# Kernel optimization log

Measured on AMD Instinct MI355X. Metric: run time of the kernel, lower is better.

Reference implementation:

```python
import jax, jax.numpy as jnp
import numpy as np

N = 128   # image_size == proj_size
C = 16    # channels
B = 1
NUM_AP = 1
AP_ANGLES = np.linspace(0.0, 0.0, NUM_AP).tolist()
APLT_ANGLES = np.linspace(0.0, np.pi / 2, 2).tolist()
EPS = 1e-5


def _conv3d(x, w, b):
    # x: [B,C,D,H,W], w: [O,I,3,3,3]
    y = jax.lax.conv_general_dilated(
        x, w, window_strides=(1, 1, 1), padding='SAME',
        dimension_numbers=('NCDHW', 'OIDHW', 'NCDHW'))
    return y + b[None, :, None, None, None]


def _instance_norm(x):
    # InstanceNorm3d, affine=False: normalize per (batch, channel) over D,H,W
    m = x.mean(axis=(2, 3, 4), keepdims=True)
    v = x.var(axis=(2, 3, 4), keepdims=True)
    return (x - m) * jax.lax.rsqrt(v + EPS)


def _resblock(x, w1, b1, w2, b2):
    out = jax.nn.relu(_instance_norm(_conv3d(x, w1, b1)))
    out = _instance_norm(_conv3d(out, w2, b2)) + x
    return jax.nn.relu(out)


def _backproject(proj):
    # proj: [B,C,A,Z,U] -> volume [B,C,Z,N,N] (parallel-beam smear-back)
    c = (N - 1) / 2.0
    ys, xs = jnp.meshgrid(jnp.arange(N, dtype=jnp.float32),
                          jnp.arange(N, dtype=jnp.float32), indexing='ij')
    vol = jnp.zeros((proj.shape[0], proj.shape[1], proj.shape[3], N, N), proj.dtype)
    for a, th in enumerate(AP_ANGLES):
        u = np.cos(th) * (ys - c) + np.sin(th) * (xs - c) + c  # [N,N] detector coord
        u0 = jnp.clip(jnp.floor(u).astype(jnp.int32), 0, N - 2)
        w = u - u0.astype(u.dtype)
        p = proj[:, :, a]                     # [B,C,Z,U]
        g = p[..., u0] * (1.0 - w) + p[..., u0 + 1] * w   # [B,C,Z,N,N]
        valid = (u >= 0.0) & (u <= N - 1.0)
        vol = vol + jnp.where(valid, g, 0.0)
    return vol / float(len(AP_ANGLES))


def _forward_project(vol):
    # vol: [B,C,Z,H,W] -> proj [B,C,A,Z,U] (line integrals per z-slice)
    c = (N - 1) / 2.0
    uu, tt = jnp.meshgrid(jnp.arange(N, dtype=jnp.float32),
                          jnp.arange(N, dtype=jnp.float32), indexing='ij')
    projs = []
    for th in APLT_ANGLES:
        y = c + (uu - c) * np.cos(th) - (tt - c) * np.sin(th)
        x = c + (uu - c) * np.sin(th) + (tt - c) * np.cos(th)
        y0 = jnp.clip(jnp.floor(y).astype(jnp.int32), 0, N - 2)
        x0 = jnp.clip(jnp.floor(x).astype(jnp.int32), 0, N - 2)
        wy = y - y0.astype(y.dtype)
        wx = x - x0.astype(x.dtype)
        g = (vol[:, :, :, y0, x0] * (1 - wy) * (1 - wx)
             + vol[:, :, :, y0 + 1, x0] * wy * (1 - wx)
             + vol[:, :, :, y0, x0 + 1] * (1 - wy) * wx
             + vol[:, :, :, y0 + 1, x0 + 1] * wy * wx)   # [B,C,Z,U,T]
        valid = (y >= 0.0) & (y <= N - 1.0) & (x >= 0.0) & (x <= N - 1.0)
        projs.append(jnp.where(valid, g, 0.0).sum(axis=-1))  # sum over ray param t
    return jnp.stack(projs, axis=2)  # [B,C,A,Z,U]


def setup_inputs() -> dict:
    key = jax.random.key(0)
    ks = jax.random.split(key, 9)
    scale = 1.0 / np.sqrt(C * 27)
    inp = {'projection_data': jax.random.normal(ks[0], (B, C, NUM_AP, N, N), jnp.float32)}
    for i, name in enumerate(['a1', 'a2', 'b1', 'b2']):
        inp['w_' + name] = jax.random.normal(ks[1 + 2 * i], (C, C, 3, 3, 3), jnp.float32) * scale
        inp['b_' + name] = jax.random.normal(ks[2 + 2 * i], (C,), jnp.float32) * 0.01
    return inp


def reference(projection_data, w_a1, b_a1, w_a2, b_a2, w_b1, b_b1, w_b2, b_b2):
    vol = _backproject(projection_data)
    vol = _resblock(vol, w_a1, b_a1, w_a2, b_a2)
    vol = _resblock(vol, w_b1, b_b1, w_b2, b_b2)
    return _forward_project(vol)
```

## Files before the change

### kernel.cpp

```cpp
#include <hip/hip_runtime.h>


typedef unsigned short u16;
typedef unsigned int   u32;
using s16x8 = __attribute__((ext_vector_type(8))) short;
using f32x4 = __attribute__((ext_vector_type(4))) float;

#define IN_ELEMS 262144
#define MN_ELEMS 4194304
#define WS_NEED  28505408ull

__device__ __forceinline__ float bf2f(u16 h) {
    union { u32 u; float f; } v; v.u = ((u32)h) << 16; return v.f;
}
__device__ __forceinline__ u16 f2bf(float f) {
    union { float f; u32 u; } v; v.f = f;
    u32 u = v.u;
    return (u16)((u + 0x7fffu + ((u >> 16) & 1u)) >> 16);
}
__device__ __forceinline__ float ldin(const void* p, int i, int bf) {
    return bf ? bf2f(((const u16*)p)[i]) : ((const float*)p)[i];
}
__device__ __forceinline__ u16 ldbf(const void* p, int i, int bf) {
    return bf ? ((const u16*)p)[i] : f2bf(((const float*)p)[i]);
}
__device__ __forceinline__ void unpack8(uint4 a, float* f) {
    u32 w[4] = {a.x, a.y, a.z, a.w};
#pragma unroll
    for (int i = 0; i < 4; i++) {
        f[2*i]   = bf2f((u16)(w[i] & 0xffff));
        f[2*i+1] = bf2f((u16)(w[i] >> 16));
    }
}
__device__ __forceinline__ void unpack4(uint2 a, float* f) {
    f[0] = bf2f((u16)(a.x & 0xffff)); f[1] = bf2f((u16)(a.x >> 16));
    f[2] = bf2f((u16)(a.y & 0xffff)); f[3] = bf2f((u16)(a.y >> 16));
}

__global__ void sentinel_k(u16* __restrict__ out, int n)
{
    int i = blockIdx.x * 256 + threadIdx.x;
    if (i < n) out[i] = 0x4640;
}

__global__ __launch_bounds__(256) void wprep_prep_k(
    const void* __restrict__ w0, const void* __restrict__ w1,
    const void* __restrict__ w2, const void* __restrict__ w3,
    const void* __restrict__ b0, const void* __restrict__ b1,
    const void* __restrict__ b2, const void* __restrict__ b3,
    const void* __restrict__ proj,
    float* __restrict__ st, int* __restrict__ flag,
    float* __restrict__ biasf, float* __restrict__ w2d,
    float* __restrict__ pz, u16* __restrict__ afrag,
    float* __restrict__ I0, u16* __restrict__ M0)
{
    const int tid = threadIdx.x;
    const u16* pp = (const u16*)w0;
    int cnt = 0;
    for (int i = 0; i < 32; i++) {
        int e = (pp[2 * i] >> 7) & 0xFF;
        if (e >= 64 && e <= 130) cnt++;
    }
    const int bf = (cnt >= 24) ? 1 : 0;
    const void* WS[4] = {w0, w1, w2, w3};
    const void* BS[4] = {b0, b1, b2, b3};
    const int b = blockIdx.x;

    if (b >= 135) {
        const int bb = b - 135;
        const int d = bb >> 2;
        const int ys = (bb & 3) * 32;
        for (int i = tid; i < 512; i += 256) {
            int y = ys + (i >> 4), c = i & 15;
            I0[(d * 128 + y) * 16 + c] = ldin(proj, c * 16384 + d * 128 + y, bf);
        }
        for (int i = tid; i < 1024; i += 256) {
            int y = ys + (i >> 5), x = (i >> 1) & 15, hh = i & 1;
            bool on = (x <= 4) | (x == 7) | (x >= 8 && x < 12);
            u32 pw[4] = {0u, 0u, 0u, 0u};
            if (on) {
#pragma unroll
                for (int j = 0; j < 4; j++) {
                    int c0 = hh * 8 + 2 * j;
                    u16 a = f2bf(ldin(proj, c0 * 16384 + d * 128 + y, bf));
                    u16 bb2 = f2bf(ldin(proj, (c0 + 1) * 16384 + d * 128 + y, bf));
                    pw[j] = (u32)a | ((u32)bb2 << 16);
                }
            }
            *(uint4*)(M0 + ((d * 128 + y) << 8) + (x << 4) + hh * 8) =
                make_uint4(pw[0], pw[1], pw[2], pw[3]);
        }
        return;
    }

    if (b < 18) {
        int gi = b * 256 + tid;
        int L = gi / 1152, r = gi - L * 1152;
        int fi = r >> 6, l = r & 63;
        int kzky = fi >> 1, grp = fi & 1;
        int kz = kzky / 3, ky = kzky % 3;
        int n = l & 15, g = l >> 4, h = g & 1, kxs = g >> 1;
        int kx = grp * 2 + kxs;
        u16 v[8];
#pragma unroll
        for (int e = 0; e < 8; e++) {
            int ci = h * 8 + e;
            v[e] = (kx <= 2) ? ldbf(WS[L], n * 432 + ci * 27 + kz * 9 + ky * 3 + kx, bf)
                             : (u16)0;
        }
#pragma unroll
        for (int e = 0; e < 8; e++) afrag[gi * 8 + e] = v[e];
    } else if (b == 18) {
        st[tid] = 0.f;
        if (tid == 0) *flag = bf;
        if (tid < 64) biasf[tid] = ldin(BS[tid >> 4], tid & 15, bf);
    } else if (b < 99) {
        int i = (b - 19) * 256 + tid;
        pz[i] = 0.f;
    } else {
        int gi = (b - 99) * 256 + tid;
        int L = gi / 2304, r = gi - L * 2304;
        int tap = r >> 8, ci = (r >> 4) & 15, co = r & 15;
        int kz = tap / 3, ky = tap % 3;
        float s = 0.f;
#pragma unroll
        for (int kx = 0; kx < 3; kx++)
            s += ldin(WS[L], (co * 16 + ci) * 27 + kz * 9 + ky * 3 + kx, bf);
        w2d[gi] = s;
    }
}

__global__ __launch_bounds__(256) void layer_k(
    const float* __restrict__ Iin, const u16* __restrict__ Min,
    const float* __restrict__ w2dL, const u16* __restrict__ afragL,
    const float* __restrict__ biasL,
    float* __restrict__ Iout, u16* __restrict__ Mout,
    float* __restrict__ st_out)
{
    __shared__ __align__(16) char smem_raw[27776];
    const int tid = threadIdx.x;

    if (blockIdx.x < 256) {
        float* smem = (float*)smem_raw;
        float* wsl  = smem;
        float* pin  = smem + 2304;
        float* sred = smem + 5670;
        const int d  = blockIdx.x >> 1;
        const int y0 = (blockIdx.x & 1) * 64;
        if (tid < 32) sred[tid] = 0.f;
        for (int i = tid; i < 2304; i += 256) wsl[i] = w2dL[i];
        for (int i = tid; i < 3168; i += 256) {
            int p = i / 1056, r = i - p * 1056;
            int row = r >> 4, c = r & 15;
            int zz = d + p - 1, gy = y0 + row - 1;
            float v = 0.f;
            if ((unsigned)zz < 128u && (unsigned)gy < 128u)
                v = Iin[(zz * 128 + gy) * 16 + c];
            pin[p * 1122 + row * 17 + c] = v;
        }
        __syncthreads();

        const int yl = tid & 63, h = tid >> 6;
        float acc[4];
#pragma unroll
        for (int cc = 0; cc < 4; cc++) acc[cc] = biasL[h * 4 + cc];
#pragma unroll
        for (int kz = 0; kz < 3; kz++) {
#pragma unroll
            for (int ky = 0; ky < 3; ky++) {
                const float* rowb = &pin[kz * 1122 + (yl + ky) * 17];
                const float* wrow = &wsl[(kz * 3 + ky) * 256 + h * 4];
#pragma unroll
                for (int ci = 0; ci < 16; ci++) {
                    float v = rowb[ci];
#pragma unroll
                    for (int cc = 0; cc < 4; cc++)
                        acc[cc] = fmaf(v, wrow[ci * 16 + cc], acc[cc]);
                }
            }
        }
        const int e = (d * 128 + y0 + yl) * 16 + h * 4;
        *(float4*)(Iout + e) = make_float4(acc[0], acc[1], acc[2], acc[3]);
        float s[4], q[4];
#pragma unroll
        for (int cc = 0; cc < 4; cc++) { s[cc] = acc[cc]; q[cc] = acc[cc] * acc[cc]; }
#pragma unroll
        for (int off = 1; off < 64; off <<= 1) {
#pragma unroll
            for (int cc = 0; cc < 4; cc++) {
                s[cc] += __shfl_down(s[cc], off, 64);
                q[cc] += __shfl_down(q[cc], off, 64);
            }
        }
        if ((tid & 63) == 0) {
#pragma unroll
            for (int cc = 0; cc < 4; cc++) {
                atomicAdd(&sred[h * 4 + cc], s[cc]);
                atomicAdd(&sred[16 + h * 4 + cc], q[cc]);
            }
        }
        __syncthreads();
        if (tid < 32) atomicAdd(&st_out[tid], 120.f * sred[tid]);
        return;
    }

    u16*   stage = (u16*)smem_raw;
    float* sred  = (float*)(smem_raw + 27648);
    const int mb = blockIdx.x - 256;
    const int z  = mb & 127;
    const int yt = mb >> 7;
    const int l = tid & 63, w = tid >> 6;
    const int n = l & 15, g = l >> 4, h = g & 1, kxs = g >> 1;
    const int y0 = yt * 16 + w * 4;
    const int y0b = yt * 16;

    if (tid < 32) sred[tid] = 0.f;

    s16x8 af[18];
#pragma unroll
    for (int fi = 0; fi < 18; fi++)
        af[fi] = *(const s16x8*)(afragL + (fi * 64 + l) * 8);
    f32x4 binit = *(const f32x4*)(biasL + g * 4);

    for (int i = tid; i < 1728; i += 256) {
        int r = i >> 5, p = i & 31;
        int kz = r / 18, yr = r - kz * 18;
        int gz = z + kz - 1, gy = y0b + yr - 1;
        uint4 v = make_uint4(0u, 0u, 0u, 0u);
        if (((unsigned)gz < 128u) & ((unsigned)gy < 128u))
            v = *(const uint4*)(Min + (((gz << 7) + gy) << 8) + p * 8);
        *(uint4*)(stage + r * 256 + p * 8) = v;
    }
    __syncthreads();

    f32x4 acc[4];
#pragma unroll
    for (int yl = 0; yl < 4; yl++) acc[yl] = binit;

    const int x0c = n + kxs - 1;
    const int x1c = x0c + 2;
    const bool v0ok = (unsigned)x0c < 16u;
    const bool v1ok = (unsigned)x1c < 16u;

#pragma unroll
    for (int kz = 0; kz < 3; kz++) {
#pragma unroll
        for (int yin = 0; yin < 6; yin++) {
            const u16* rowp = stage + (kz * 18 + (w << 2) + yin) * 256 + h * 8;
            uint4 q0 = make_uint4(0u, 0u, 0u, 0u);
            uint4 q1 = make_uint4(0u, 0u, 0u, 0u);
            if (v0ok) q0 = *(const uint4*)(rowp + (x0c << 4));
            if (v1ok) q1 = *(const uint4*)(rowp + (x1c << 4));
            s16x8 f0 = __builtin_bit_cast(s16x8, q0);
            s16x8 f1 = __builtin_bit_cast(s16x8, q1);
#pragma unroll
            for (int ky = 0; ky < 3; ky++) {
                const int yl = yin - ky;
                if (yl >= 0 && yl < 4) {
                    acc[yl] = __builtin_amdgcn_mfma_f32_16x16x32_bf16(af[(kz * 3 + ky) * 2],     f0, acc[yl], 0, 0, 0);
                    acc[yl] = __builtin_amdgcn_mfma_f32_16x16x32_bf16(af[(kz * 3 + ky) * 2 + 1], f1, acc[yl], 0, 0, 0);
                }
            }
        }
    }

    const float inc = (((n >> 2) & 1) == 0) ? 1.f : 0.f;
    float sr[4] = {0.f, 0.f, 0.f, 0.f}, qr[4] = {0.f, 0.f, 0.f, 0.f};
#pragma unroll
    for (int yl = 0; yl < 4; yl++) {
        const int gy = y0 + yl;
        u32 lo = (u32)f2bf(acc[yl][0]) | ((u32)f2bf(acc[yl][1]) << 16);
        u32 hi = (u32)f2bf(acc[yl][2]) | ((u32)f2bf(acc[yl][3]) << 16);
        *(uint2*)(Mout + (((z << 7) + gy) << 8) + (n << 4) + g * 4) = make_uint2(lo, hi);
#pragma unroll
        for (int r = 0; r < 4; r++) {
            sr[r] += inc * acc[yl][r];
            qr[r] = fmaf(inc * acc[yl][r], acc[yl][r], qr[r]);
        }
    }
#pragma unroll
    for (int off = 1; off < 16; off <<= 1) {
#pragma unroll
        for (int r = 0; r < 4; r++) {
            sr[r] += __shfl_down(sr[r], off, 16);
            qr[r] += __shfl_down(qr[r], off, 16);
        }
    }
    __syncthreads();
    if (n == 0) {
#pragma unroll
        for (int r = 0; r < 4; r++) {
            atomicAdd(&sred[g * 4 + r], sr[r]);
            atomicAdd(&sred[16 + g * 4 + r], qr[r]);
        }
    }
    __syncthreads();
    if (tid < 32) atomicAdd(&st_out[tid], sred[tid]);
}

template <int RES>
__global__ __launch_bounds__(256) void norm_k(
    const float* __restrict__ Iraw, const u16* __restrict__ Mraw,
    const void* __restrict__ proj, const float* __restrict__ stL,
    const int* __restrict__ flagp,
    float* __restrict__ Iout, u16* __restrict__ Mout)
{
    __shared__ float sA[32];
    const int bf = *flagp;
    const int d  = blockIdx.x >> 2;
    const int ys = (blockIdx.x & 3) * 32;
    const int tid = threadIdx.x;
    if (tid < 32) {
        const float inv = 1.f / 2097152.f;
        int c = tid & 15;
        float m = stL[c] * inv;
        sA[tid] = (tid < 16) ? m : rsqrtf(stL[16 + c] * inv - m * m + 1e-5f);
    }
    __syncthreads();
    for (int i = tid; i < 512; i += 256) {
        int y = ys + (i >> 4), c = i & 15;
        float res = RES ? ldin(proj, c * 16384 + d * 128 + y, bf) : 0.f;
        float v = fmaxf((Iraw[(d * 128 + y) * 16 + c] - sA[c]) * sA[16 + c] + res, 0.f);
        Iout[(d * 128 + y) * 16 + c] = v;
    }
    for (int i = tid; i < 1024; i += 256) {
        int y = ys + (i >> 5), x = (i >> 1) & 15, hh = i & 1;
        bool realc = (x < 4) | (x >= 8 && x < 12);
        bool ghost = (x == 4) | (x == 7);
        u32 pw[4] = {0u, 0u, 0u, 0u};
        if (realc | ghost) {
            float f[8];
            if (realc) {
                uint4 raw = *(const uint4*)(Mraw + ((d * 128 + y) << 8) + (x << 4) + hh * 8);
                unpack8(raw, f);
            } else {
#pragma unroll
                for (int j = 0; j < 8; j++)
                    f[j] = Iraw[(d * 128 + y) * 16 + hh * 8 + j];
            }
            float vals[8];
#pragma unroll
            for (int j = 0; j < 8; j++) {
                int c = hh * 8 + j;
                float res = RES ? ldin(proj, c * 16384 + d * 128 + y, bf) : 0.f;
                vals[j] = fmaxf((f[j] - sA[c]) * sA[16 + c] + res, 0.f);
            }
#pragma unroll
            for (int j = 0; j < 4; j++)
                pw[j] = (u32)f2bf(vals[2*j]) | ((u32)f2bf(vals[2*j+1]) << 16);
        }
        *(uint4*)(Mout + ((d * 128 + y) << 8) + (x << 4) + hh * 8) =
            make_uint4(pw[0], pw[1], pw[2], pw[3]);
    }
}

__global__ __launch_bounds__(256) void fproj1_k(
    const float* __restrict__ I4, const float* __restrict__ IXB,
    const u16* __restrict__ M4, const u16* __restrict__ MXB,
    const float* __restrict__ stL, const int* __restrict__ flagp,
    void* __restrict__ out,
    float* __restrict__ P, float* __restrict__ PS, float* __restrict__ P0)
{
    __shared__ float sA[32];
    const int bf = *flagp;
    const int d = blockIdx.x >> 1;
    const int half = blockIdx.x & 1;
    const int tid = threadIdx.x;
    if (tid < 32) {
        const float inv = 1.f / 2097152.f;
        int c = tid & 15;
        float m = stL[c] * inv;
        sA[tid] = (tid < 16) ? m : rsqrtf(stL[16 + c] * inv - m * m + 1e-5f);
    }
    __syncthreads();

    const int yl = tid & 63, y = half * 64 + yl;
    const int h = tid >> 6, c0 = h * 4;

    float v2d[4], row[4];
    {
        const int e = (d * 128 + y) * 16 + c0;
        float4 a = *(const float4*)(I4 + e);
        float4 x = *(const float4*)(IXB + e);
        float ia[4] = {a.x, a.y, a.z, a.w};
        float xa[4] = {x.x, x.y, x.z, x.w};
#pragma unroll
        for (int cc = 0; cc < 4; cc++) {
            int c = c0 + cc;
            v2d[cc] = fmaxf((ia[cc] - sA[c]) * sA[16 + c] + xa[cc], 0.f);
            row[cc] = 120.f * v2d[cc];
        }
    }
    float colp[8][4];
#pragma unroll
    for (int j = 0; j < 8; j++) {
        const int m = (j < 4) ? j : j + 4;
        const int e = ((d * 128 + y) << 8) + (m << 4) + c0;
        float f4[4], fx[4];
        unpack4(*(const uint2*)(M4 + e), f4);
        unpack4(*(const uint2*)(MXB + e), fx);
#pragma unroll
        for (int cc = 0; cc < 4; cc++) {
            int c = c0 + cc;
            float v = fmaxf((f4[cc] - sA[c]) * sA[16 + c] + fx[cc], 0.f);
            row[cc] += v;
            colp[j][cc] = v;
        }
    }
#pragma unroll
    for (int cc = 0; cc < 4; cc++) {
        int oi = ((c0 + cc) * 2) * 16384 + d * 128 + y;
        if (bf) ((u16*)out)[oi] = f2bf(row[cc]); else ((float*)out)[oi] = row[cc];
    }
#pragma unroll
    for (int off = 1; off < 64; off <<= 1) {
#pragma unroll
        for (int cc = 0; cc < 4; cc++) {
            v2d[cc] += __shfl_down(v2d[cc], off, 64);
#pragma unroll
            for (int j = 0; j < 8; j++)
                colp[j][cc] += __shfl_down(colp[j][cc], off, 64);
        }
    }
    if (yl == 0) {
#pragma unroll
        for (int cc = 0; cc < 4; cc++) {
            atomicAdd(&PS[d * 16 + c0 + cc], v2d[cc]);
#pragma unroll
            for (int j = 0; j < 8; j++)
                atomicAdd(&P[(d * 8 + j) * 16 + c0 + cc], colp[j][cc]);
            if (half == 0) P0[d * 16 + c0 + cc] = colp[0][cc];
        }
    }
}

__global__ __launch_bounds__(256) void fproj2_k(
    const float* __restrict__ P, const float* __restrict__ PS,
    const float* __restrict__ P0, const int* __restrict__ flagp,
    void* __restrict__ out)
{
    const int bf = *flagp;
    const int d = blockIdx.x;
    const int tid = threadIdx.x;
    for (int i = tid; i < 2048; i += 256) {
        int c = i >> 7, u = i & 127;
        float v;
        if (u == 0)        v = P0[d * 16 + c];
        else if (u < 4)    v = P[(d * 8 + u) * 16 + c];
        else if (u >= 124) v = P[(d * 8 + (u - 120)) * 16 + c];
        else               v = PS[d * 16 + c];
        int oi = (c * 2 + 1) * 16384 + d * 128 + u;
        if (bf) ((u16*)out)[oi] = f2bf(v); else ((float*)out)[oi] = v;
    }
}

extern "C" void kernel_launch(void* const* d_in, const int* in_sizes, int n_in,
                              void* d_out, int out_size, void* d_ws, size_t ws_size,
                              hipStream_t stream)
{
    if (ws_size < WS_NEED) {
        sentinel_k<<<(out_size + 255) / 256, 256, 0, stream>>>((u16*)d_out, out_size);
        return;
    }
    const void* proj = d_in[0];
    const void* w1 = d_in[1]; const void* b1 = d_in[2];
    const void* w2 = d_in[3]; const void* b2 = d_in[4];
    const void* w3 = d_in[5]; const void* b3 = d_in[6];
    const void* w4 = d_in[7]; const void* b4 = d_in[8];

    float* I_A  = (float*)d_ws;
    float* I_B  = I_A + IN_ELEMS;
    float* I_XB = I_B + IN_ELEMS;
    u16*   M_A  = (u16*)(I_XB + IN_ELEMS);
    u16*   M_B  = M_A + MN_ELEMS;
    u16*   M_XB = M_B + MN_ELEMS;
    float* st    = (float*)(M_XB + MN_ELEMS);
    int*   flag  = (int*)(st + 256);
    float* biasf = (float*)(flag + 16);
    float* w2d   = biasf + 64;
    float* P     = w2d + 9216;
    float* PS    = P + 16384;
    float* P0    = PS + 2048;
    u16*   afrag = (u16*)(P0 + 2048);

    wprep_prep_k<<<647, 256, 0, stream>>>(w1, w2, w3, w4, b1, b2, b3, b4, proj,
                                          st, flag, biasf, w2d, P, afrag, I_A, M_A);

    dim3 lg(1280), cb(256);
    layer_k<<<lg, cb, 0, stream>>>(I_A, M_A, w2d + 0,    afrag + 0,     biasf + 0,  I_B, M_B, st + 0);
    norm_k<0><<<512, cb, 0, stream>>>(I_B, M_B, proj, st + 0, flag, I_A, M_A);
    layer_k<<<lg, cb, 0, stream>>>(I_A, M_A, w2d + 2304, afrag + 9216,  biasf + 16, I_B, M_B, st + 64);
    norm_k<1><<<512, cb, 0, stream>>>(I_B, M_B, proj, st + 64, flag, I_XB, M_XB);
    layer_k<<<lg, cb, 0, stream>>>(I_XB, M_XB, w2d + 4608, afrag + 18432, biasf + 32, I_B, M_B, st + 128);
    norm_k<0><<<512, cb, 0, stream>>>(I_B, M_B, proj, st + 128, flag, I_A, M_A);
    layer_k<<<lg, cb, 0, stream>>>(I_A, M_A, w2d + 6912, afrag + 27648, biasf + 48, I_B, M_B, st + 192);
    fproj1_k<<<256, cb, 0, stream>>>(I_B, I_XB, M_B, M_XB, st + 192, flag, d_out, P, PS, P0);
    fproj2_k<<<128, cb, 0, stream>>>(P, PS, P0, flag, d_out);
}
```

Before: 214.3 us.

## Fuse instance-norm/ReLU/residual into the next conv layer's input staging

Removes the three standalone norm_k launches and instead applies the previous layer's instance-norm, residual add and ReLU while each conv block stages its input halo. The residual block input is written out to the XB buffers from the center plane of the third layer. This saves launches and a full read-write pass over the activations per norm. In exchange, halo elements are normalized redundantly, proj is re-read per halo element, and the buffer ping-pong is reordered.

```diff
diff --git a/kernel.cpp b/kernel.cpp
--- a/kernel.cpp
+++ b/kernel.cpp
@@ -130,32 +130,54 @@
     }
 }
 
+template <int NORM, int RES, int WXB>
 __global__ __launch_bounds__(256) void layer_k(
     const float* __restrict__ Iin, const u16* __restrict__ Min,
+    const void* __restrict__ proj, const float* __restrict__ stP,
+    const int* __restrict__ flagp,
     const float* __restrict__ w2dL, const u16* __restrict__ afragL,
     const float* __restrict__ biasL,
     float* __restrict__ Iout, u16* __restrict__ Mout,
+    float* __restrict__ IXB, u16* __restrict__ MXB,
     float* __restrict__ st_out)
 {
-    __shared__ __align__(16) char smem_raw[27776];
+    __shared__ __align__(16) char smem_raw[27904];
     const int tid = threadIdx.x;
+    const int bf = RES ? *flagp : 0;
 
     if (blockIdx.x < 256) {
         float* smem = (float*)smem_raw;
         float* wsl  = smem;
         float* pin  = smem + 2304;
         float* sred = smem + 5670;
+        float* sA   = smem + 5702;
         const int d  = blockIdx.x >> 1;
         const int y0 = (blockIdx.x & 1) * 64;
-        if (tid < 32) sred[tid] = 0.f;
+        if (tid < 32) {
+            sred[tid] = 0.f;
+            if (NORM) {
+                const float inv = 1.f / 2097152.f;
+                int c = tid & 15;
+                float m = stP[c] * inv;
+                sA[tid] = (tid < 16) ? m : rsqrtf(stP[16 + c] * inv - m * m + 1e-5f);
+            }
+        }
         for (int i = tid; i < 2304; i += 256) wsl[i] = w2dL[i];
+        if (NORM) __syncthreads();
         for (int i = tid; i < 3168; i += 256) {
             int p = i / 1056, r = i - p * 1056;
             int row = r >> 4, c = r & 15;
             int zz = d + p - 1, gy = y0 + row - 1;
             float v = 0.f;
-            if ((unsigned)zz < 128u && (unsigned)gy < 128u)
+            if ((unsigned)zz < 128u && (unsigned)gy < 128u) {
                 v = Iin[(zz * 128 + gy) * 16 + c];
+                if (NORM) {
+                    float res = RES ? ldin(proj, c * 16384 + zz * 128 + gy, bf) : 0.f;
+                    v = fmaxf((v - sA[c]) * sA[16 + c] + res, 0.f);
+                }
+                if (WXB && p == 1 && row >= 1 && row <= 64)
+                    IXB[(d * 128 + gy) * 16 + c] = v;
+            }
             pin[p * 1122 + row * 17 + c] = v;
         }
         __syncthreads();
@@ -206,6 +228,7 @@
 
     u16*   stage = (u16*)smem_raw;
     float* sred  = (float*)(smem_raw + 27648);
+    float* sA    = (float*)(smem_raw + 27776);
     const int mb = blockIdx.x - 256;
     const int z  = mb & 127;
     const int yt = mb >> 7;
@@ -214,23 +237,65 @@
     const int y0 = yt * 16 + w * 4;
     const int y0b = yt * 16;
 
-    if (tid < 32) sred[tid] = 0.f;
-
-    s16x8 af[18];
-#pragma unroll
-    for (int fi = 0; fi < 18; fi++)
-        af[fi] = *(const s16x8*)(afragL + (fi * 64 + l) * 8);
-    f32x4 binit = *(const f32x4*)(biasL + g * 4);
+    if (tid < 32) {
+        sred[tid] = 0.f;
+        if (NORM) {
+            const float inv = 1.f / 2097152.f;
+            int c = tid & 15;
+            float m = stP[c] * inv;
+            sA[tid] = (tid < 16) ? m : rsqrtf(stP[16 + c] * inv - m * m + 1e-5f);
+        }
+    }
+    if (NORM) __syncthreads();
 
     for (int i = tid; i < 1728; i += 256) {
         int r = i >> 5, p = i & 31;
         int kz = r / 18, yr = r - kz * 18;
         int gz = z + kz - 1, gy = y0b + yr - 1;
         uint4 v = make_uint4(0u, 0u, 0u, 0u);
-        if (((unsigned)gz < 128u) & ((unsigned)gy < 128u))
-            v = *(const uint4*)(Min + (((gz << 7) + gy) << 8) + p * 8);
+        bool inb = ((unsigned)gz < 128u) & ((unsigned)gy < 128u);
+        if (!NORM) {
+            if (inb) v = *(const uint4*)(Min + (((gz << 7) + gy) << 8) + p * 8);
+        } else {
+            int x = p >> 1, hh = p & 1;
+            bool realc = (x < 4) | (x >= 8 && x < 12);
+            bool ghost = (x == 4) | (x == 7);
+            if (inb & (realc | ghost)) {
+                float f[8];
+                if (realc) {
+                    uint4 raw = *(const uint4*)(Min + (((gz << 7) + gy) << 8) + p * 8);
+                    unpack8(raw, f);
+                } else {
+                    const float* ip = Iin + ((gz * 128 + gy) * 16 + hh * 8);
+                    float4 a  = *(const float4*)(ip);
+                    float4 b2 = *(const float4*)(ip + 4);
+                    f[0] = a.x;  f[1] = a.y;  f[2] = a.z;  f[3] = a.w;
+                    f[4] = b2.x; f[5] = b2.y; f[6] = b2.z; f[7] = b2.w;
+                }
+                float vals[8];
+#pragma unroll
+                for (int j = 0; j < 8; j++) {
+                    int c = hh * 8 + j;
+                    float res = RES ? ldin(proj, c * 16384 + gz * 128 + gy, bf) : 0.f;
+                    vals[j] = fmaxf((f[j] - sA[c]) * sA[16 + c] + res, 0.f);
+                }
+                u32 pw[4];
+#pragma unroll
+                for (int j = 0; j < 4; j++)
+                    pw[j] = (u32)f2bf(vals[2*j]) | ((u32)f2bf(vals[2*j+1]) << 16);
+                v = make_uint4(pw[0], pw[1], pw[2], pw[3]);
+            }
+            if (WXB && kz == 1 && yr >= 1 && yr <= 16)
+                *(uint4*)(MXB + (((z << 7) + gy) << 8) + p * 8) = v;
+        }
         *(uint4*)(stage + r * 256 + p * 8) = v;
     }
+
+    s16x8 af[18];
+#pragma unroll
+    for (int fi = 0; fi < 18; fi++)
+        af[fi] = *(const s16x8*)(afragL + (fi * 64 + l) * 8);
+    f32x4 binit = *(const f32x4*)(biasL + g * 4);
     __syncthreads();
 
     f32x4 acc[4];
@@ -296,62 +361,6 @@
     }
     __syncthreads();
     if (tid < 32) atomicAdd(&st_out[tid], sred[tid]);
-}
-
-template <int RES>
-__global__ __launch_bounds__(256) void norm_k(
-    const float* __restrict__ Iraw, const u16* __restrict__ Mraw,
-    const void* __restrict__ proj, const float* __restrict__ stL,
-    const int* __restrict__ flagp,
-    float* __restrict__ Iout, u16* __restrict__ Mout)
-{
-    __shared__ float sA[32];
-    const int bf = *flagp;
-    const int d  = blockIdx.x >> 2;
-    const int ys = (blockIdx.x & 3) * 32;
-    const int tid = threadIdx.x;
-    if (tid < 32) {
-        const float inv = 1.f / 2097152.f;
-        int c = tid & 15;
-        float m = stL[c] * inv;
-        sA[tid] = (tid < 16) ? m : rsqrtf(stL[16 + c] * inv - m * m + 1e-5f);
-    }
-    __syncthreads();
-    for (int i = tid; i < 512; i += 256) {
-        int y = ys + (i >> 4), c = i & 15;
-        float res = RES ? ldin(proj, c * 16384 + d * 128 + y, bf) : 0.f;
-        float v = fmaxf((Iraw[(d * 128 + y) * 16 + c] - sA[c]) * sA[16 + c] + res, 0.f);
-        Iout[(d * 128 + y) * 16 + c] = v;
-    }
-    for (int i = tid; i < 1024; i += 256) {
-        int y = ys + (i >> 5), x = (i >> 1) & 15, hh = i & 1;
-        bool realc = (x < 4) | (x >= 8 && x < 12);
-        bool ghost = (x == 4) | (x == 7);
-        u32 pw[4] = {0u, 0u, 0u, 0u};
-        if (realc | ghost) {
-            float f[8];
-            if (realc) {
-                uint4 raw = *(const uint4*)(Mraw + ((d * 128 + y) << 8) + (x << 4) + hh * 8);
-                unpack8(raw, f);
-            } else {
-#pragma unroll
-                for (int j = 0; j < 8; j++)
-                    f[j] = Iraw[(d * 128 + y) * 16 + hh * 8 + j];
-            }
-            float vals[8];
-#pragma unroll
-            for (int j = 0; j < 8; j++) {
-                int c = hh * 8 + j;
-                float res = RES ? ldin(proj, c * 16384 + d * 128 + y, bf) : 0.f;
-                vals[j] = fmaxf((f[j] - sA[c]) * sA[16 + c] + res, 0.f);
-            }
-#pragma unroll
-            for (int j = 0; j < 4; j++)
-                pw[j] = (u32)f2bf(vals[2*j]) | ((u32)f2bf(vals[2*j+1]) << 16);
-        }
-        *(uint4*)(Mout + ((d * 128 + y) << 8) + (x << 4) + hh * 8) =
-            make_uint4(pw[0], pw[1], pw[2], pw[3]);
-    }
 }
 
 __global__ __launch_bounds__(256) void fproj1_k(
@@ -487,13 +496,18 @@
                                           st, flag, biasf, w2d, P, afrag, I_A, M_A);
 
     dim3 lg(1280), cb(256);
-    layer_k<<<lg, cb, 0, stream>>>(I_A, M_A, w2d + 0,    afrag + 0,     biasf + 0,  I_B, M_B, st + 0);
-    norm_k<0><<<512, cb, 0, stream>>>(I_B, M_B, proj, st + 0, flag, I_A, M_A);
-    layer_k<<<lg, cb, 0, stream>>>(I_A, M_A, w2d + 2304, afrag + 9216,  biasf + 16, I_B, M_B, st + 64);
-    norm_k<1><<<512, cb, 0, stream>>>(I_B, M_B, proj, st + 64, flag, I_XB, M_XB);
-    layer_k<<<lg, cb, 0, stream>>>(I_XB, M_XB, w2d + 4608, afrag + 18432, biasf + 32, I_B, M_B, st + 128);
-    norm_k<0><<<512, cb, 0, stream>>>(I_B, M_B, proj, st + 128, flag, I_A, M_A);
-    layer_k<<<lg, cb, 0, stream>>>(I_A, M_A, w2d + 6912, afrag + 27648, biasf + 48, I_B, M_B, st + 192);
-    fproj1_k<<<256, cb, 0, stream>>>(I_B, I_XB, M_B, M_XB, st + 192, flag, d_out, P, PS, P0);
+    layer_k<0,0,0><<<lg, cb, 0, stream>>>(I_A, M_A, proj, st, flag,
+                                          w2d + 0,    afrag + 0,     biasf + 0,
+                                          I_B, M_B, nullptr, nullptr, st + 0);
+    layer_k<1,0,0><<<lg, cb, 0, stream>>>(I_B, M_B, proj, st + 0, flag,
+                                          w2d + 2304, afrag + 9216,  biasf + 16,
+                                          I_A, M_A, nullptr, nullptr, st + 64);
+    layer_k<1,1,1><<<lg, cb, 0, stream>>>(I_A, M_A, proj, st + 64, flag,
+                                          w2d + 4608, afrag + 18432, biasf + 32,
+                                          I_B, M_B, I_XB, M_XB, st + 128);
+    layer_k<1,0,0><<<lg, cb, 0, stream>>>(I_B, M_B, proj, st + 128, flag,
+                                          w2d + 6912, afrag + 27648, biasf + 48,
+                                          I_A, M_A, nullptr, nullptr, st + 192);
+    fproj1_k<<<256, cb, 0, stream>>>(I_A, I_XB, M_A, M_XB, st + 192, flag, d_out, P, PS, P0);
     fproj2_k<<<128, cb, 0, stream>>>(P, PS, P0, flag, d_out);
 }
```

Result: no change. 211.4 us (-1.3%).
